# Kernel optimization log

Measured on AMD Instinct MI355X. Metric: run time of the kernel, lower is better.

The kernel has to match this reference:

```python
import math
import jax, jax.numpy as jnp
import numpy as np

T = 4096
D_MODEL = 1024
NUM_HEADS = 16
HEAD_DIM = D_MODEL // NUM_HEADS


def setup_inputs() -> dict:
    key = jax.random.key(0)
    k_x, k_wqkv, k_wproj = jax.random.split(key, 3)
    # match eqx.nn.Linear init scale: U(-1/sqrt(in), 1/sqrt(in)); randn*small works too,
    # but keep magnitudes reasonable so softmax isn't saturated.
    s_in = 1.0 / math.sqrt(D_MODEL)
    x = jax.random.normal(k_x, (T, D_MODEL), dtype=jnp.float32)
    W_qkv = jax.random.normal(k_wqkv, (3 * D_MODEL, D_MODEL), dtype=jnp.float32) * s_in
    b_qkv = jnp.zeros((3 * D_MODEL,), dtype=jnp.float32)
    W_proj = jax.random.normal(k_wproj, (D_MODEL, D_MODEL), dtype=jnp.float32) * s_in
    b_proj = jnp.zeros((D_MODEL,), dtype=jnp.float32)
    return {"x": x, "W_qkv": W_qkv, "b_qkv": b_qkv, "W_proj": W_proj, "b_proj": b_proj}


def reference(x, W_qkv, b_qkv, W_proj, b_proj):
    T_, C = x.shape  # (seq, d_model)
    H, hd = NUM_HEADS, HEAD_DIM
    # c_attn: eqx Linear computes W @ x + b per token -> x @ W.T + b
    qkv = x @ W_qkv.T + b_qkv  # (T, 3C)
    q, k, v = jnp.split(qkv, 3, axis=1)
    # (T, C) -> (H, T, hd)
    q = q.reshape(T_, H, hd).swapaxes(0, 1)
    k = k.reshape(T_, H, hd).swapaxes(0, 1)
    v = v.reshape(T_, H, hd).swapaxes(0, 1)
    scores = jnp.einsum("htd,hsd->hts", q, k) / math.sqrt(hd)  # (H, T, T)
    causal = jnp.tril(jnp.ones((T_, T_), dtype=bool))
    scores = jnp.where(causal, scores, -jnp.inf)
    attn = jax.nn.softmax(scores, axis=-1)
    y = jnp.einsum("hts,hsd->htd", attn, v)  # (H, T, hd)
    y = y.swapaxes(0, 1).reshape(T_, C)
    y = y @ W_proj.T + b_proj
    return y
```

## Files before the change

### kernel.cpp

```cpp
#include <hip/hip_runtime.h>
#include <math.h>
#include <string.h>

#define T_SEQ 4096
#define DM 1024
#define NH 16
#define HD 64

typedef short s8v __attribute__((ext_vector_type(8)));
typedef float f4v __attribute__((ext_vector_type(4)));

__device__ inline unsigned short f2bf(float f) {
    unsigned u; memcpy(&u, &f, 4);
    u = u + 0x7fffu + ((u >> 16) & 1u);
    return (unsigned short)(u >> 16);
}

__device__ inline float bf2f(unsigned short s) {
    unsigned u = (unsigned)s << 16;
    float f; memcpy(&f, &u, 4);
    return f;
}

__device__ inline float exp2fn(float x) {
#if __has_builtin(__builtin_amdgcn_exp2f)
    return __builtin_amdgcn_exp2f(x);
#else
    return exp2f(x);
#endif
}

__device__ inline void gld_lds16(const void* g, void* l) {
    __builtin_amdgcn_global_load_lds(
        (const __attribute__((address_space(1))) void*)g,
        (__attribute__((address_space(3))) void*)l, 16, 0, 0);
}

__global__ __launch_bounds__(256)
void cvt3(const float* __restrict__ i0, unsigned short* __restrict__ o0, int n0,
          const float* __restrict__ i1, unsigned short* __restrict__ o1, int n1,
          const float* __restrict__ i2, unsigned short* __restrict__ o2, int n2) {
    int i = blockIdx.x * 256 + threadIdx.x;
    const float* in; unsigned short* out; int j;
    if (i < n0)           { in = i0; out = o0; j = i; }
    else if (i < n0 + n1) { in = i1; out = o1; j = i - n0; }
    else if (i < n0 + n1 + n2) { in = i2; out = o2; j = i - n0 - n1; }
    else return;
    const float4* p = (const float4*)(in + (size_t)j * 8);
    float4 a = p[0], b = p[1];
    unsigned short o[8] = {f2bf(a.x), f2bf(a.y), f2bf(a.z), f2bf(a.w),
                           f2bf(b.x), f2bf(b.y), f2bf(b.z), f2bf(b.w)};
    uint4 pk; memcpy(&pk, o, 16);
    *(uint4*)(out + (size_t)j * 8) = pk;
}

template<int MODE, int TM, int TN, int WR, int WC>
__global__ __launch_bounds__(WR * WC * 64, 1)
void gemm_tile(const unsigned short* __restrict__ A, const unsigned short* __restrict__ B,
               const float* __restrict__ bias, void* __restrict__ Cout,
               unsigned short* __restrict__ qbuf, unsigned short* __restrict__ kbuf2,
               unsigned short* __restrict__ vT,
               int M, int N, int K, int nbx, int patchw, int patchh) {
    constexpr int W  = WR * WC;
    constexpr int MF = TM / WR / 16;
    constexpr int NF = TN / WC / 16;
    constexpr int NGA = TM / 16, NGB = TN / 16, NG = NGA + NGB;
    __shared__ __align__(16) short As[2][TM * 32];
    __shared__ __align__(16) short Bs[2][TN * 32];
    const int tid = threadIdx.x;
    const int w = tid >> 6, lane = tid & 63;
    const int wr = w / WC, wc = w % WC;
    const int l15 = lane & 15, quad = lane >> 4;

    const int bl = blockIdx.x;
    const int xcd = bl & 7, ii = bl >> 3;
    const int pxn = nbx / patchw;
    const int bx = (xcd % pxn) * patchw + ii % patchw;
    const int by = (xcd / pxn) * patchh + ii / patchw;
    const int m0 = by * TM, n0 = bx * TN;

    f4v acc[MF][NF];
    #pragma unroll
    for (int i = 0; i < MF; ++i)
        #pragma unroll
        for (int j = 0; j < NF; ++j) acc[i][j] = (f4v){0.f, 0.f, 0.f, 0.f};

    auto stage = [&](int buf, int k0) {
        for (int g = w; g < NG; g += W) {
            const unsigned short* src;
            short* dst;
            if (g < NGA) {
                src = A + (size_t)(m0 + g * 16 + l15) * K + quad * 8 + k0;
                dst = &As[buf][g * 512];
            } else {
                src = B + (size_t)(n0 + (g - NGA) * 16 + l15) * K + quad * 8 + k0;
                dst = &Bs[buf][(g - NGA) * 512];
            }
            gld_lds16(src, dst);
        }
    };
    auto compute = [&](int buf) {
        s8v af[MF], bfr[NF];
        #pragma unroll
        for (int i = 0; i < MF; ++i)
            af[i] = *(const s8v*)&As[buf][((wr * MF + i) * 64 + lane) * 8];
        #pragma unroll
        for (int j = 0; j < NF; ++j)
            bfr[j] = *(const s8v*)&Bs[buf][((wc * NF + j) * 64 + lane) * 8];
        #pragma unroll
        for (int i = 0; i < MF; ++i)
            #pragma unroll
            for (int j = 0; j < NF; ++j)
                acc[i][j] = __builtin_amdgcn_mfma_f32_16x16x32_bf16(af[i], bfr[j], acc[i][j], 0, 0, 0);
    };

    stage(0, 0);
    __syncthreads();
    for (int k0 = 0; k0 < K; k0 += 64) {
        stage(1, k0 + 32);
        compute(0);
        __syncthreads();
        if (k0 + 64 < K) stage(0, k0 + 64);
        compute(1);
        __syncthreads();
    }

    float bj[NF];
    #pragma unroll
    for (int j = 0; j < NF; ++j) bj[j] = bias[n0 + wc * (TN / WC) + j * 16 + l15];

    if (MODE == 2) {
        #pragma unroll
        for (int j = 0; j < NF; ++j) {
            const int ccol = n0 + wc * (TN / WC) + j * 16;
            if (ccol >= 2 * DM) {
                const int hh = (ccol - 2 * DM) >> 6;
                const int ob = (ccol & 63) >> 4;
                #pragma unroll
                for (int i = 0; i < MF; ++i) {
                    const int tile = (m0 + wr * (TM / WR)) / 64 + (i >> 2);
                    const int it = i & 3;
                    unsigned short o[4];
                    #pragma unroll
                    for (int rg = 0; rg < 4; ++rg) o[rg] = f2bf(acc[i][j][rg] + bj[j]);
                    unsigned long long pk; memcpy(&pk, o, 8);
                    size_t off = (size_t)hh * 262144 + (size_t)tile * 4096
                               + (size_t)((ob * 2 + (it >> 1)) * 64 + lane) * 8 + (it & 1) * 4;
                    *(unsigned long long*)&vT[off] = pk;
                }
            } else {
                unsigned short* dst = (ccol < DM) ? qbuf : kbuf2;
                const int col = (ccol < DM) ? (ccol + l15) : (ccol - DM + l15);
                #pragma unroll
                for (int i = 0; i < MF; ++i) {
                    #pragma unroll
                    for (int rg = 0; rg < 4; ++rg) {
                        int row = m0 + wr * (TM / WR) + i * 16 + quad * 4 + rg;
                        dst[(size_t)row * DM + col] = f2bf(acc[i][j][rg] + bj[j]);
                    }
                }
            }
        }
    } else {
        #pragma unroll
        for (int i = 0; i < MF; ++i) {
            #pragma unroll
            for (int rg = 0; rg < 4; ++rg) {
                int row = m0 + wr * (TM / WR) + i * 16 + quad * 4 + rg;
                #pragma unroll
                for (int j = 0; j < NF; ++j) {
                    int col = n0 + wc * (TN / WC) + j * 16 + l15;
                    ((float*)Cout)[(size_t)row * N + col] = acc[i][j][rg] + bj[j];
                }
            }
        }
    }
}

__device__ __forceinline__ void soft_step(f4v* st, bool diag, int qloc, int quad,
                                          float& lr, s8v& pf0, s8v& pf1) {
    const float C2  = 0.1803368851f;
    const float MC2 = 12.0f * 0.1803368851f;
    float sv[4][4];
    #pragma unroll
    for (int kb = 0; kb < 4; ++kb)
        #pragma unroll
        for (int rg = 0; rg < 4; ++rg) {
            float s = st[kb][rg];
            if (diag && (kb * 16 + quad * 4 + rg > qloc)) s = -3.0e38f;
            float t = exp2fn(fmaf(s, C2, -MC2));
            sv[kb][rg] = t;
            lr += t;
        }
    int pk[4][2];
    #pragma unroll
    for (int kb = 0; kb < 4; ++kb) {
        unsigned u0 = __float_as_uint(sv[kb][0]) + 0x8000u;
        unsigned u1 = __float_as_uint(sv[kb][1]) + 0x8000u;
        unsigned u2 = __float_as_uint(sv[kb][2]) + 0x8000u;
        unsigned u3 = __float_as_uint(sv[kb][3]) + 0x8000u;
        pk[kb][0] = (int)__builtin_amdgcn_perm(u1, u0, 0x07060302);
        pk[kb][1] = (int)__builtin_amdgcn_perm(u3, u2, 0x07060302);
    }
    int4 a = {pk[0][0], pk[0][1], pk[1][0], pk[1][1]};
    int4 b = {pk[2][0], pk[2][1], pk[3][0], pk[3][1]};
    memcpy(&pf0, &a, 16);
    memcpy(&pf1, &b, 16);
}

__global__ __launch_bounds__(256, 3)
void attn_mfma7(const unsigned short* __restrict__ qb,
                const unsigned short* __restrict__ kbf,
                const unsigned short* __restrict__ vT,
                unsigned short* __restrict__ y0,
                unsigned short* __restrict__ y1,
                unsigned short* __restrict__ y2,
                float* __restrict__ lsum) {
    const int b = blockIdx.x;
    const int par = b % 3;
    const int idx = b / 3;
    const int h = idx & 15, a = idx >> 4;
    const int tid = threadIdx.x;
    const int w = tid >> 6, lane = tid & 63;
    const int quad = lane >> 4, l15 = lane & 15;
    const int cq = h * HD;
    unsigned short* ypar = (par == 0) ? y0 : (par == 1) ? y1 : y2;
    float* lpar = lsum + ((size_t)par * NH + h) * T_SEQ;
    const unsigned short* vbase = vT + (size_t)h * 262144;

    __shared__ short KB[2][4096];
    __shared__ short VTs[2][4096];
    __shared__ short QB[8192];

    for (int ph = 0; ph < 2; ++ph) {
        const int qt = ph ? (31 - a) : a;
        const int q0 = qt * 128;
        const int kmax = 2 * qt + 1;
        const int nk = (kmax >= par) ? (kmax - par) / 3 + 1 : 0;
        const int kt0 = par * 64;

        __syncthreads();
        #pragma unroll
        for (int rr = 0; rr < 4; ++rr) {
            int ch = rr * 256 + tid;
            int qg = ch >> 7, hf = (ch >> 6) & 1, ln = ch & 63;
            gld_lds16(qb + (size_t)(q0 + qg * 16 + (ln & 15)) * DM + cq + hf * 32 + ((ln >> 4) << 3),
                      &QB[(ch & ~63) * 8]);
        }
        if (nk > 0) {
            #pragma unroll
            for (int rr = 0; rr < 2; ++rr) {
                int ch = rr * 256 + tid;
                int blk = ch >> 7, hf = (ch >> 6) & 1, ln = ch & 63;
                gld_lds16(kbf + (size_t)(kt0 + blk * 16 + (ln & 15)) * DM + cq + hf * 32 + ((ln >> 4) << 3),
                          &KB[0][(ch & ~63) * 8]);
                gld_lds16(vbase + (size_t)(kt0 >> 6) * 4096 + (size_t)ch * 8,
                          &VTs[0][(ch & ~63) * 8]);
            }
        }
        __syncthreads();

        s8v qf[2][2];
        #pragma unroll
        for (int g = 0; g < 2; ++g)
            #pragma unroll
            for (int hf = 0; hf < 2; ++hf)
                qf[g][hf] = *(const s8v*)&QB[((((g * 4 + w) * 2 + hf) * 64) + lane) * 8];

        f4v O0[4], O1[4];
        #pragma unroll
        for (int ob = 0; ob < 4; ++ob) {
            O0[ob] = (f4v){0.f, 0.f, 0.f, 0.f};
            O1[ob] = (f4v){0.f, 0.f, 0.f, 0.f};
        }
        float lr0 = 0.f, lr1 = 0.f;

        for (int i = 0; i < nk; ++i) {
            const int kt = par + 3 * i;
            const int p = i & 1;
            const bool g0a = (kt <= 2 * qt);
            const bool m0 = (kt == 2 * qt);
            const bool m1 = (kt == 2 * qt + 1);
            if (i < nk - 1) {
                const int k1 = kt0 + (i + 1) * 192;
                #pragma unroll
                for (int rr = 0; rr < 2; ++rr) {
                    int ch = rr * 256 + tid;
                    int blk = ch >> 7, hf = (ch >> 6) & 1, ln = ch & 63;
                    gld_lds16(kbf + (size_t)(k1 + blk * 16 + (ln & 15)) * DM + cq
                                  + hf * 32 + ((ln >> 4) << 3),
                              &KB[p ^ 1][(ch & ~63) * 8]);
                    gld_lds16(vbase + (size_t)(k1 >> 6) * 4096 + (size_t)ch * 8,
                              &VTs[p ^ 1][(ch & ~63) * 8]);
                }
            }

            f4v st0[4], st1[4];
            #pragma unroll
            for (int kb = 0; kb < 4; ++kb) {
                s8v k0f = *(const s8v*)&KB[p][((kb * 2 + 0) * 64 + lane) * 8];
                s8v k1f = *(const s8v*)&KB[p][((kb * 2 + 1) * 64 + lane) * 8];
                f4v c1 = (f4v){0.f, 0.f, 0.f, 0.f};
                c1 = __builtin_amdgcn_mfma_f32_16x16x32_bf16(k0f, qf[1][0], c1, 0, 0, 0);
                c1 = __builtin_amdgcn_mfma_f32_16x16x32_bf16(k1f, qf[1][1], c1, 0, 0, 0);
                st1[kb] = c1;
                if (g0a) {
                    f4v c0 = (f4v){0.f, 0.f, 0.f, 0.f};
                    c0 = __builtin_amdgcn_mfma_f32_16x16x32_bf16(k0f, qf[0][0], c0, 0, 0, 0);
                    c0 = __builtin_amdgcn_mfma_f32_16x16x32_bf16(k1f, qf[0][1], c0, 0, 0, 0);
                    st0[kb] = c0;
                }
            }

            s8v pf10, pf11, pf00, pf01;
            soft_step(st1, m1, w * 16 + l15, quad, lr1, pf10, pf11);
            if (g0a) soft_step(st0, m0, w * 16 + l15, quad, lr0, pf00, pf01);

            #pragma unroll
            for (int ob = 0; ob < 4; ++ob) {
                s8v v0f = *(const s8v*)&VTs[p][((ob * 2 + 0) * 64 + lane) * 8];
                s8v v1f = *(const s8v*)&VTs[p][((ob * 2 + 1) * 64 + lane) * 8];
                O1[ob] = __builtin_amdgcn_mfma_f32_16x16x32_bf16(v0f, pf10, O1[ob], 0, 0, 0);
                O1[ob] = __builtin_amdgcn_mfma_f32_16x16x32_bf16(v1f, pf11, O1[ob], 0, 0, 0);
                if (g0a) {
                    O0[ob] = __builtin_amdgcn_mfma_f32_16x16x32_bf16(v0f, pf00, O0[ob], 0, 0, 0);
                    O0[ob] = __builtin_amdgcn_mfma_f32_16x16x32_bf16(v1f, pf01, O0[ob], 0, 0, 0);
                }
            }
            __syncthreads();
        }

        lr0 += __shfl_xor(lr0, 16); lr0 += __shfl_xor(lr0, 32);
        lr1 += __shfl_xor(lr1, 16); lr1 += __shfl_xor(lr1, 32);
        #pragma unroll
        for (int g = 0; g < 2; ++g) {
            const f4v* O = g ? O1 : O0;
            int qrow = q0 + g * 64 + w * 16 + l15;
            size_t ybase = (size_t)qrow * DM + cq;
            #pragma unroll
            for (int ob = 0; ob < 4; ++ob) {
                unsigned short o[4];
                #pragma unroll
                for (int rg = 0; rg < 4; ++rg) o[rg] = f2bf(O[ob][rg]);
                unsigned long long pk; memcpy(&pk, o, 8);
                *(unsigned long long*)&ypar[ybase + ob * 16 + quad * 4] = pk;
            }
            if (quad == 0) lpar[qrow] = g ? lr1 : lr0;
        }
    }
}

__global__ __launch_bounds__(256)
void attn_combine3(const unsigned short* __restrict__ y0,
                   const unsigned short* __restrict__ y1,
                   const unsigned short* __restrict__ y2,
                   const float* __restrict__ lsum,
                   unsigned short* __restrict__ yout) {
    int i = blockIdx.x * 256 + threadIdx.x;
    int t = i >> 7, d8 = i & 127;
    int h = d8 >> 3;
    float l = lsum[(size_t)h * T_SEQ + t]
            + lsum[((size_t)NH + h) * T_SEQ + t]
            + lsum[((size_t)2 * NH + h) * T_SEQ + t];
    float inv = 1.f / l;
    size_t off = (size_t)t * DM + d8 * 8;
    uint4 ua = *(const uint4*)(y0 + off);
    uint4 ub = *(const uint4*)(y1 + off);
    uint4 uc = *(const uint4*)(y2 + off);
    const unsigned short* pa = (const unsigned short*)&ua;
    const unsigned short* pb = (const unsigned short*)&ub;
    const unsigned short* pc = (const unsigned short*)&uc;
    unsigned short o[8];
    #pragma unroll
    for (int k = 0; k < 8; ++k)
        o[k] = f2bf((bf2f(pa[k]) + bf2f(pb[k]) + bf2f(pc[k])) * inv);
    uint4 pk; memcpy(&pk, o, 16);
    *(uint4*)(yout + off) = pk;
}

extern "C" void kernel_launch(void* const* d_in, const int* in_sizes, int n_in,
                              void* d_out, int out_size, void* d_ws, size_t ws_size,
                              hipStream_t stream) {
    const float* x     = (const float*)d_in[0];
    const float* Wqkv  = (const float*)d_in[1];
    const float* bqkv  = (const float*)d_in[2];
    const float* Wproj = (const float*)d_in[3];
    const float* bproj = (const float*)d_in[4];
    float* out = (float*)d_out;

    char* ws = (char*)d_ws;
    unsigned short* qbuf  = (unsigned short*)(ws);
    unsigned short* kbuf  = (unsigned short*)(ws + ( 8u << 20));
    unsigned short* vTb   = (unsigned short*)(ws + (16u << 20));
    unsigned short* yattb = (unsigned short*)(ws + (24u << 20));
    unsigned short* wprjb = (unsigned short*)(ws + (32u << 20));
    float*          lsum  = (float*)         (ws + (34u << 20));
    unsigned short* xb    = (unsigned short*)(ws + (35u << 20));
    unsigned short* wqkvb = (unsigned short*)(ws + (43u << 20));
    unsigned short* y0p   = (unsigned short*)(ws + (35u << 20));
    unsigned short* y1p   = (unsigned short*)(ws + (43u << 20));
    unsigned short* y2p   = (unsigned short*)(ws + (51u << 20));

    {
        int n0 = T_SEQ * DM / 8, n1 = 3 * DM * DM / 8, n2 = DM * DM / 8;
        cvt3<<<dim3((n0 + n1 + n2 + 255) / 256), dim3(256), 0, stream>>>(
            x, xb, n0, Wqkv, wqkvb, n1, Wproj, wprjb, n2);
    }
    gemm_tile<2, 256, 192, 2, 4><<<dim3(256), dim3(512), 0, stream>>>(
        xb, wqkvb, bqkv, nullptr, qbuf, kbuf, vTb, T_SEQ, 3 * DM, DM, 16, 8, 4);
    attn_mfma7<<<dim3(768), dim3(256), 0, stream>>>(qbuf, kbuf, vTb, y0p, y1p, y2p, lsum);
    attn_combine3<<<dim3(T_SEQ * DM / 8 / 256), dim3(256), 0, stream>>>(y0p, y1p, y2p, lsum, yattb);
    gemm_tile<0, 128, 128, 2, 2><<<dim3(256), dim3(256), 0, stream>>>(
        yattb, wprjb, bproj, out, nullptr, nullptr, nullptr, T_SEQ, DM, DM, 8, 4, 8);
}
```

Before: 214.5 us.

## Restructure GEMM into triple-buffered four-phase pipeline with explicit waitcnt scheduling

Replaces the double-buffered GEMM main loop with a three-stage LDS ring. Each K-step is split into four phases, and in each phase every wave issues one global-to-LDS load for step s+2 while running a slice of its MFMAs. Explicit vmcnt/lgkmcnt waits, s_barrier, sched_barrier and setprio replace the generic __syncthreads, so loads overlap more deeply with math. The QKV GEMM tile also grows to 256x256 (192 blocks instead of 256), and occupancy hints change. This uses more LDS and barriers per step, and depends on hand-tuned wait counts being correct.

Measured after the change: 222.9 us. 3.9% more time.

```diff
diff --git a/kernel.cpp b/kernel.cpp
--- a/kernel.cpp
+++ b/kernel.cpp
@@ -54,19 +54,22 @@
     *(uint4*)(out + (size_t)j * 8) = pk;
 }
 
-template<int MODE, int TM, int TN, int WR, int WC>
-__global__ __launch_bounds__(WR * WC * 64, 1)
-void gemm_tile(const unsigned short* __restrict__ A, const unsigned short* __restrict__ B,
-               const float* __restrict__ bias, void* __restrict__ Cout,
-               unsigned short* __restrict__ qbuf, unsigned short* __restrict__ kbuf2,
-               unsigned short* __restrict__ vT,
-               int M, int N, int K, int nbx, int patchw, int patchh) {
+template<int MODE, int TM, int TN, int WR, int WC, int OCC>
+__global__ __launch_bounds__(WR * WC * 64, OCC)
+void gemm_8ph(const unsigned short* __restrict__ A, const unsigned short* __restrict__ B,
+              const float* __restrict__ bias, void* __restrict__ Cout,
+              unsigned short* __restrict__ qbuf, unsigned short* __restrict__ kbuf2,
+              unsigned short* __restrict__ vT,
+              int M, int N, int K, int nbx, int patchw, int patchh) {
     constexpr int W  = WR * WC;
     constexpr int MF = TM / WR / 16;
     constexpr int NF = TN / WC / 16;
-    constexpr int NGA = TM / 16, NGB = TN / 16, NG = NGA + NGB;
-    __shared__ __align__(16) short As[2][TM * 32];
-    __shared__ __align__(16) short Bs[2][TN * 32];
+    constexpr int MFP = MF / 4;
+    constexpr int NGA = TM / 16, NGB = TN / 16;
+    static_assert(NGA + NGB == 4 * W, "one stage-load per wave per phase");
+    static_assert(MF % 4 == 0, "4 phases per K-step");
+    __shared__ __align__(16) short As[3][NGA * 512];
+    __shared__ __align__(16) short Bs[3][NGB * 512];
     const int tid = threadIdx.x;
     const int w = tid >> 6, lane = tid & 63;
     const int wr = w / WC, wc = w % WC;
@@ -85,44 +88,54 @@
         #pragma unroll
         for (int j = 0; j < NF; ++j) acc[i][j] = (f4v){0.f, 0.f, 0.f, 0.f};
 
-    auto stage = [&](int buf, int k0) {
-        for (int g = w; g < NG; g += W) {
-            const unsigned short* src;
-            short* dst;
-            if (g < NGA) {
-                src = A + (size_t)(m0 + g * 16 + l15) * K + quad * 8 + k0;
-                dst = &As[buf][g * 512];
-            } else {
-                src = B + (size_t)(n0 + (g - NGA) * 16 + l15) * K + quad * 8 + k0;
-                dst = &Bs[buf][(g - NGA) * 512];
-            }
-            gld_lds16(src, dst);
-        }
+    auto stage_group = [&](int buf, int g, int k0) {
+        if (g < NGA)
+            gld_lds16(A + (size_t)(m0 + g * 16 + l15) * K + quad * 8 + k0,
+                      &As[buf][g * 512]);
+        else
+            gld_lds16(B + (size_t)(n0 + (g - NGA) * 16 + l15) * K + quad * 8 + k0,
+                      &Bs[buf][(g - NGA) * 512]);
     };
-    auto compute = [&](int buf) {
-        s8v af[MF], bfr[NF];
-        #pragma unroll
-        for (int i = 0; i < MF; ++i)
-            af[i] = *(const s8v*)&As[buf][((wr * MF + i) * 64 + lane) * 8];
-        #pragma unroll
-        for (int j = 0; j < NF; ++j)
-            bfr[j] = *(const s8v*)&Bs[buf][((wc * NF + j) * 64 + lane) * 8];
-        #pragma unroll
-        for (int i = 0; i < MF; ++i)
-            #pragma unroll
-            for (int j = 0; j < NF; ++j)
-                acc[i][j] = __builtin_amdgcn_mfma_f32_16x16x32_bf16(af[i], bfr[j], acc[i][j], 0, 0, 0);
-    };
-
-    stage(0, 0);
-    __syncthreads();
-    for (int k0 = 0; k0 < K; k0 += 64) {
-        stage(1, k0 + 32);
-        compute(0);
-        __syncthreads();
-        if (k0 + 64 < K) stage(0, k0 + 64);
-        compute(1);
-        __syncthreads();
+
+    const int nstep = K >> 5;
+    #pragma unroll
+    for (int s = 0; s < 2; ++s)
+        #pragma unroll
+        for (int p = 0; p < 4; ++p)
+            stage_group(s, p * W + w, s * 32);
+
+    for (int s = 0; s < nstep; ++s) {
+        const int cb = s % 3, pb = (s + 2) % 3;
+        if (s + 1 < nstep) asm volatile("s_waitcnt vmcnt(4)" ::: "memory");
+        else               asm volatile("s_waitcnt vmcnt(0)" ::: "memory");
+        __builtin_amdgcn_s_barrier();
+        asm volatile("" ::: "memory");
+        s8v bfr[NF];
+        #pragma unroll
+        for (int p = 0; p < 4; ++p) {
+            if (s + 2 < nstep) stage_group(pb, p * W + w, (s + 2) * 32);
+            s8v af[MFP];
+            #pragma unroll
+            for (int i = 0; i < MFP; ++i)
+                af[i] = *(const s8v*)&As[cb][((wr * MF + p * MFP + i) * 64 + lane) * 8];
+            if (p == 0) {
+                #pragma unroll
+                for (int j = 0; j < NF; ++j)
+                    bfr[j] = *(const s8v*)&Bs[cb][((wc * NF + j) * 64 + lane) * 8];
+            }
+            asm volatile("s_waitcnt lgkmcnt(0)" ::: "memory");
+            __builtin_amdgcn_sched_barrier(0);
+            __builtin_amdgcn_s_setprio(1);
+            #pragma unroll
+            for (int i = 0; i < MFP; ++i)
+                #pragma unroll
+                for (int j = 0; j < NF; ++j)
+                    acc[p * MFP + i][j] = __builtin_amdgcn_mfma_f32_16x16x32_bf16(
+                        af[i], bfr[j], acc[p * MFP + i][j], 0, 0, 0);
+            __builtin_amdgcn_s_setprio(0);
+            __builtin_amdgcn_s_barrier();
+            asm volatile("" ::: "memory");
+        }
     }
 
     float bj[NF];
@@ -406,10 +419,10 @@
         cvt3<<<dim3((n0 + n1 + n2 + 255) / 256), dim3(256), 0, stream>>>(
             x, xb, n0, Wqkv, wqkvb, n1, Wproj, wprjb, n2);
     }
-    gemm_tile<2, 256, 192, 2, 4><<<dim3(256), dim3(512), 0, stream>>>(
-        xb, wqkvb, bqkv, nullptr, qbuf, kbuf, vTb, T_SEQ, 3 * DM, DM, 16, 8, 4);
+    gemm_8ph<2, 256, 256, 2, 4, 2><<<dim3(192), dim3(512), 0, stream>>>(
+        xb, wqkvb, bqkv, nullptr, qbuf, kbuf, vTb, T_SEQ, 3 * DM, DM, 12, 6, 4);
     attn_mfma7<<<dim3(768), dim3(256), 0, stream>>>(qbuf, kbuf, vTb, y0p, y1p, y2p, lsum);
     attn_combine3<<<dim3(T_SEQ * DM / 8 / 256), dim3(256), 0, stream>>>(y0p, y1p, y2p, lsum, yattb);
-    gemm_tile<0, 128, 128, 2, 2><<<dim3(256), dim3(256), 0, stream>>>(
+    gemm_8ph<0, 128, 128, 2, 2, 3><<<dim3(256), dim3(256), 0, stream>>>(
         yattb, wprjb, bproj, out, nullptr, nullptr, nullptr, T_SEQ, DM, DM, 8, 4, 8);
 }
```

## Fuse attention partial combine and normalization into output projection GEMM A-load

Applied to the files above, without the earlier changes.

Removes the separate combine kernel that summed three partial attention outputs and divided by the summed softmax denominators. The projection GEMM, in a new MODE 3, instead stages all three partial A tiles into LDS and forms the combined, normalized bf16 fragment before each MFMA. The per-row denominators are read once per 64-wide k-step, which lines up with one head because HD is 64. This drops a kernel launch and a full write and re-read of the combined activation. In exchange the GEMM triples its A loads and A-side LDS, and adds VALU work to its inner loop, repeated for every column tile.

After: 246.9 us. 1.15x slower.

```diff
diff --git a/kernel.cpp b/kernel.cpp
--- a/kernel.cpp
+++ b/kernel.cpp
@@ -56,7 +56,9 @@
 
 template<int MODE, int TM, int TN, int WR, int WC>
 __global__ __launch_bounds__(WR * WC * 64, 1)
-void gemm_tile(const unsigned short* __restrict__ A, const unsigned short* __restrict__ B,
+void gemm_tile(const unsigned short* __restrict__ A, const unsigned short* __restrict__ A1,
+               const unsigned short* __restrict__ A2, const float* __restrict__ lsm,
+               const unsigned short* __restrict__ B,
                const float* __restrict__ bias, void* __restrict__ Cout,
                unsigned short* __restrict__ qbuf, unsigned short* __restrict__ kbuf2,
                unsigned short* __restrict__ vT,
@@ -65,8 +67,9 @@
     constexpr int MF = TM / WR / 16;
     constexpr int NF = TN / WC / 16;
     constexpr int NGA = TM / 16, NGB = TN / 16, NG = NGA + NGB;
-    __shared__ __align__(16) short As[2][TM * 32];
-    __shared__ __align__(16) short Bs[2][TN * 32];
+    constexpr int NP = (MODE == 3) ? 3 : 1;
+    __shared__ __align__(16) short As[2][NP][NGA * 512];
+    __shared__ __align__(16) short Bs[2][NGB * 512];
     const int tid = threadIdx.x;
     const int w = tid >> 6, lane = tid & 63;
     const int wr = w / WC, wc = w % WC;
@@ -87,23 +90,36 @@
 
     auto stage = [&](int buf, int k0) {
         for (int g = w; g < NG; g += W) {
-            const unsigned short* src;
-            short* dst;
             if (g < NGA) {
-                src = A + (size_t)(m0 + g * 16 + l15) * K + quad * 8 + k0;
-                dst = &As[buf][g * 512];
+                size_t off = (size_t)(m0 + g * 16 + l15) * K + quad * 8 + k0;
+                gld_lds16(A + off, &As[buf][0][g * 512]);
+                if (MODE == 3) {
+                    gld_lds16(A1 + off, &As[buf][1][g * 512]);
+                    gld_lds16(A2 + off, &As[buf][2][g * 512]);
+                }
             } else {
-                src = B + (size_t)(n0 + (g - NGA) * 16 + l15) * K + quad * 8 + k0;
-                dst = &Bs[buf][(g - NGA) * 512];
-            }
-            gld_lds16(src, dst);
+                gld_lds16(B + (size_t)(n0 + (g - NGA) * 16 + l15) * K + quad * 8 + k0,
+                          &Bs[buf][(g - NGA) * 512]);
+            }
         }
     };
-    auto compute = [&](int buf) {
+    auto compute = [&](int buf, const float* inv) {
         s8v af[MF], bfr[NF];
         #pragma unroll
-        for (int i = 0; i < MF; ++i)
-            af[i] = *(const s8v*)&As[buf][((wr * MF + i) * 64 + lane) * 8];
+        for (int i = 0; i < MF; ++i) {
+            if (MODE == 3) {
+                const unsigned short* p0 = (const unsigned short*)&As[buf][0][((wr * MF + i) * 64 + lane) * 8];
+                const unsigned short* p1 = (const unsigned short*)&As[buf][1][((wr * MF + i) * 64 + lane) * 8];
+                const unsigned short* p2 = (const unsigned short*)&As[buf][2][((wr * MF + i) * 64 + lane) * 8];
+                unsigned short o[8];
+                #pragma unroll
+                for (int e = 0; e < 8; ++e)
+                    o[e] = f2bf((bf2f(p0[e]) + bf2f(p1[e]) + bf2f(p2[e])) * inv[i]);
+                memcpy(&af[i], o, 16);
+            } else {
+                af[i] = *(const s8v*)&As[buf][0][((wr * MF + i) * 64 + lane) * 8];
+            }
+        }
         #pragma unroll
         for (int j = 0; j < NF; ++j)
             bfr[j] = *(const s8v*)&Bs[buf][((wc * NF + j) * 64 + lane) * 8];
@@ -117,11 +133,23 @@
     stage(0, 0);
     __syncthreads();
     for (int k0 = 0; k0 < K; k0 += 64) {
+        float inv[MF];
+        if (MODE == 3) {
+            const int hk = k0 >> 6;
+            #pragma unroll
+            for (int i = 0; i < MF; ++i) {
+                int row = m0 + (wr * MF + i) * 16 + l15;
+                float l = lsm[((size_t)(0 * NH + hk)) * T_SEQ + row]
+                        + lsm[((size_t)(1 * NH + hk)) * T_SEQ + row]
+                        + lsm[((size_t)(2 * NH + hk)) * T_SEQ + row];
+                inv[i] = 1.f / l;
+            }
+        }
         stage(1, k0 + 32);
-        compute(0);
+        compute(0, inv);
         __syncthreads();
         if (k0 + 64 < K) stage(0, k0 + 64);
-        compute(1);
+        compute(1, inv);
         __syncthreads();
     }
 
@@ -350,34 +378,6 @@
     }
 }
 
-__global__ __launch_bounds__(256)
-void attn_combine3(const unsigned short* __restrict__ y0,
-                   const unsigned short* __restrict__ y1,
-                   const unsigned short* __restrict__ y2,
-                   const float* __restrict__ lsum,
-                   unsigned short* __restrict__ yout) {
-    int i = blockIdx.x * 256 + threadIdx.x;
-    int t = i >> 7, d8 = i & 127;
-    int h = d8 >> 3;
-    float l = lsum[(size_t)h * T_SEQ + t]
-            + lsum[((size_t)NH + h) * T_SEQ + t]
-            + lsum[((size_t)2 * NH + h) * T_SEQ + t];
-    float inv = 1.f / l;
-    size_t off = (size_t)t * DM + d8 * 8;
-    uint4 ua = *(const uint4*)(y0 + off);
-    uint4 ub = *(const uint4*)(y1 + off);
-    uint4 uc = *(const uint4*)(y2 + off);
-    const unsigned short* pa = (const unsigned short*)&ua;
-    const unsigned short* pb = (const unsigned short*)&ub;
-    const unsigned short* pc = (const unsigned short*)&uc;
-    unsigned short o[8];
-    #pragma unroll
-    for (int k = 0; k < 8; ++k)
-        o[k] = f2bf((bf2f(pa[k]) + bf2f(pb[k]) + bf2f(pc[k])) * inv);
-    uint4 pk; memcpy(&pk, o, 16);
-    *(uint4*)(yout + off) = pk;
-}
-
 extern "C" void kernel_launch(void* const* d_in, const int* in_sizes, int n_in,
                               void* d_out, int out_size, void* d_ws, size_t ws_size,
                               hipStream_t stream) {
@@ -392,7 +392,6 @@
     unsigned short* qbuf  = (unsigned short*)(ws);
     unsigned short* kbuf  = (unsigned short*)(ws + ( 8u << 20));
     unsigned short* vTb   = (unsigned short*)(ws + (16u << 20));
-    unsigned short* yattb = (unsigned short*)(ws + (24u << 20));
     unsigned short* wprjb = (unsigned short*)(ws + (32u << 20));
     float*          lsum  = (float*)         (ws + (34u << 20));
     unsigned short* xb    = (unsigned short*)(ws + (35u << 20));
@@ -407,9 +406,10 @@
             x, xb, n0, Wqkv, wqkvb, n1, Wproj, wprjb, n2);
     }
     gemm_tile<2, 256, 192, 2, 4><<<dim3(256), dim3(512), 0, stream>>>(
-        xb, wqkvb, bqkv, nullptr, qbuf, kbuf, vTb, T_SEQ, 3 * DM, DM, 16, 8, 4);
+        xb, nullptr, nullptr, nullptr, wqkvb, bqkv, nullptr,
+        qbuf, kbuf, vTb, T_SEQ, 3 * DM, DM, 16, 8, 4);
     attn_mfma7<<<dim3(768), dim3(256), 0, stream>>>(qbuf, kbuf, vTb, y0p, y1p, y2p, lsum);
-    attn_combine3<<<dim3(T_SEQ * DM / 8 / 256), dim3(256), 0, stream>>>(y0p, y1p, y2p, lsum, yattb);
-    gemm_tile<0, 128, 128, 2, 2><<<dim3(256), dim3(256), 0, stream>>>(
-        yattb, wprjb, bproj, out, nullptr, nullptr, nullptr, T_SEQ, DM, DM, 8, 4, 8);
-}
+    gemm_tile<3, 128, 128, 2, 2><<<dim3(256), dim3(256), 0, stream>>>(
+        y0p, y1p, y2p, lsum, wprjb, bproj, out,
+        nullptr, nullptr, nullptr, T_SEQ, DM, DM, 8, 4, 8);
+}
```

## Split attention KV range into two partitions with 8-wave blocks

Applied to the files above, without the earlier changes.

Changes the split-K attention from three key-tile partitions with 256-thread blocks (each wave handling two 16-row query groups) to two partitions with 512-thread blocks, where each of 8 waves owns one 16-row query group. Each block now strides key tiles by 2 instead of 3, and the combine kernel sums two partial outputs instead of three. The intent is to reduce partial-output traffic and combine work while keeping per-wave register pressure lower. The trade-off is fewer blocks, a longer serial key loop per block, and idle waves on masked diagonal tiles.

After: 212.2 us (median of 2 runs). About the same (-1.0%).

```diff
diff --git a/kernel.cpp b/kernel.cpp
--- a/kernel.cpp
+++ b/kernel.cpp
@@ -208,23 +208,22 @@
     memcpy(&pf1, &b, 16);
 }
 
-__global__ __launch_bounds__(256, 3)
-void attn_mfma7(const unsigned short* __restrict__ qb,
-                const unsigned short* __restrict__ kbf,
-                const unsigned short* __restrict__ vT,
-                unsigned short* __restrict__ y0,
-                unsigned short* __restrict__ y1,
-                unsigned short* __restrict__ y2,
-                float* __restrict__ lsum) {
+__global__ __launch_bounds__(512, 4)
+void attn_mfma2p(const unsigned short* __restrict__ qb,
+                 const unsigned short* __restrict__ kbf,
+                 const unsigned short* __restrict__ vT,
+                 unsigned short* __restrict__ y0,
+                 unsigned short* __restrict__ y1,
+                 float* __restrict__ lsum) {
     const int b = blockIdx.x;
-    const int par = b % 3;
-    const int idx = b / 3;
+    const int par = b >> 8;
+    const int idx = b & 255;
     const int h = idx & 15, a = idx >> 4;
     const int tid = threadIdx.x;
     const int w = tid >> 6, lane = tid & 63;
     const int quad = lane >> 4, l15 = lane & 15;
     const int cq = h * HD;
-    unsigned short* ypar = (par == 0) ? y0 : (par == 1) ? y1 : y2;
+    unsigned short* ypar = par ? y1 : y0;
     float* lpar = lsum + ((size_t)par * NH + h) * T_SEQ;
     const unsigned short* vbase = vT + (size_t)h * 262144;
 
@@ -232,148 +231,118 @@
     __shared__ short VTs[2][4096];
     __shared__ short QB[8192];
 
+    const bool lo = (w < 4);
+    const int qloc = (w & 3) * 16 + l15;
+
     for (int ph = 0; ph < 2; ++ph) {
         const int qt = ph ? (31 - a) : a;
         const int q0 = qt * 128;
-        const int kmax = 2 * qt + 1;
-        const int nk = (kmax >= par) ? (kmax - par) / 3 + 1 : 0;
+        const int nk = qt + 1;
         const int kt0 = par * 64;
 
         __syncthreads();
         #pragma unroll
-        for (int rr = 0; rr < 4; ++rr) {
-            int ch = rr * 256 + tid;
+        for (int rr = 0; rr < 2; ++rr) {
+            int ch = rr * 512 + tid;
             int qg = ch >> 7, hf = (ch >> 6) & 1, ln = ch & 63;
             gld_lds16(qb + (size_t)(q0 + qg * 16 + (ln & 15)) * DM + cq + hf * 32 + ((ln >> 4) << 3),
                       &QB[(ch & ~63) * 8]);
         }
-        if (nk > 0) {
+        {
+            int ch = tid;
+            int blk = ch >> 7, hf = (ch >> 6) & 1, ln = ch & 63;
+            gld_lds16(kbf + (size_t)(kt0 + blk * 16 + (ln & 15)) * DM + cq + hf * 32 + ((ln >> 4) << 3),
+                      &KB[0][(ch & ~63) * 8]);
+            gld_lds16(vbase + (size_t)(kt0 >> 6) * 4096 + (size_t)ch * 8,
+                      &VTs[0][(ch & ~63) * 8]);
+        }
+        __syncthreads();
+
+        s8v qf[2];
+        #pragma unroll
+        for (int hf = 0; hf < 2; ++hf)
+            qf[hf] = *(const s8v*)&QB[(((w * 2 + hf) * 64) + lane) * 8];
+
+        f4v O[4];
+        #pragma unroll
+        for (int ob = 0; ob < 4; ++ob) O[ob] = (f4v){0.f, 0.f, 0.f, 0.f};
+        float lr = 0.f;
+
+        for (int i = 0; i < nk; ++i) {
+            const int kt = par + 2 * i;
+            const int p = i & 1;
+            const bool diag = lo ? (kt == 2 * qt) : (kt == 2 * qt + 1);
+            const bool skip = lo && (kt == 2 * qt + 1);
+            if (i < nk - 1) {
+                const int k1 = kt0 + (i + 1) * 128;
+                int ch = tid;
+                int blk = ch >> 7, hf = (ch >> 6) & 1, ln = ch & 63;
+                gld_lds16(kbf + (size_t)(k1 + blk * 16 + (ln & 15)) * DM + cq
+                              + hf * 32 + ((ln >> 4) << 3),
+                          &KB[p ^ 1][(ch & ~63) * 8]);
+                gld_lds16(vbase + (size_t)(k1 >> 6) * 4096 + (size_t)ch * 8,
+                          &VTs[p ^ 1][(ch & ~63) * 8]);
+            }
+
+            if (!skip) {
+                f4v st[4];
+                #pragma unroll
+                for (int kb = 0; kb < 4; ++kb) {
+                    s8v k0f = *(const s8v*)&KB[p][((kb * 2 + 0) * 64 + lane) * 8];
+                    s8v k1f = *(const s8v*)&KB[p][((kb * 2 + 1) * 64 + lane) * 8];
+                    f4v c = (f4v){0.f, 0.f, 0.f, 0.f};
+                    c = __builtin_amdgcn_mfma_f32_16x16x32_bf16(k0f, qf[0], c, 0, 0, 0);
+                    c = __builtin_amdgcn_mfma_f32_16x16x32_bf16(k1f, qf[1], c, 0, 0, 0);
+                    st[kb] = c;
+                }
+                s8v pf0, pf1;
+                soft_step(st, diag, qloc, quad, lr, pf0, pf1);
+                #pragma unroll
+                for (int ob = 0; ob < 4; ++ob) {
+                    s8v v0f = *(const s8v*)&VTs[p][((ob * 2 + 0) * 64 + lane) * 8];
+                    s8v v1f = *(const s8v*)&VTs[p][((ob * 2 + 1) * 64 + lane) * 8];
+                    O[ob] = __builtin_amdgcn_mfma_f32_16x16x32_bf16(v0f, pf0, O[ob], 0, 0, 0);
+                    O[ob] = __builtin_amdgcn_mfma_f32_16x16x32_bf16(v1f, pf1, O[ob], 0, 0, 0);
+                }
+            }
+            __syncthreads();
+        }
+
+        lr += __shfl_xor(lr, 16); lr += __shfl_xor(lr, 32);
+        const int qrow = q0 + w * 16 + l15;
+        const size_t ybase = (size_t)qrow * DM + cq;
+        #pragma unroll
+        for (int ob = 0; ob < 4; ++ob) {
+            unsigned short o[4];
             #pragma unroll
-            for (int rr = 0; rr < 2; ++rr) {
-                int ch = rr * 256 + tid;
-                int blk = ch >> 7, hf = (ch >> 6) & 1, ln = ch & 63;
-                gld_lds16(kbf + (size_t)(kt0 + blk * 16 + (ln & 15)) * DM + cq + hf * 32 + ((ln >> 4) << 3),
-                          &KB[0][(ch & ~63) * 8]);
-                gld_lds16(vbase + (size_t)(kt0 >> 6) * 4096 + (size_t)ch * 8,
-                          &VTs[0][(ch & ~63) * 8]);
-            }
-        }
-        __syncthreads();
-
-        s8v qf[2][2];
-        #pragma unroll
-        for (int g = 0; g < 2; ++g)
-            #pragma unroll
-            for (int hf = 0; hf < 2; ++hf)
-                qf[g][hf] = *(const s8v*)&QB[((((g * 4 + w) * 2 + hf) * 64) + lane) * 8];
-
-        f4v O0[4], O1[4];
-        #pragma unroll
-        for (int ob = 0; ob < 4; ++ob) {
-            O0[ob] = (f4v){0.f, 0.f, 0.f, 0.f};
-            O1[ob] = (f4v){0.f, 0.f, 0.f, 0.f};
-        }
-        float lr0 = 0.f, lr1 = 0.f;
-
-        for (int i = 0; i < nk; ++i) {
-            const int kt = par + 3 * i;
-            const int p = i & 1;
-            const bool g0a = (kt <= 2 * qt);
-            const bool m0 = (kt == 2 * qt);
-            const bool m1 = (kt == 2 * qt + 1);
-            if (i < nk - 1) {
-                const int k1 = kt0 + (i + 1) * 192;
-                #pragma unroll
-                for (int rr = 0; rr < 2; ++rr) {
-                    int ch = rr * 256 + tid;
-                    int blk = ch >> 7, hf = (ch >> 6) & 1, ln = ch & 63;
-                    gld_lds16(kbf + (size_t)(k1 + blk * 16 + (ln & 15)) * DM + cq
-                                  + hf * 32 + ((ln >> 4) << 3),
-                              &KB[p ^ 1][(ch & ~63) * 8]);
-                    gld_lds16(vbase + (size_t)(k1 >> 6) * 4096 + (size_t)ch * 8,
-                              &VTs[p ^ 1][(ch & ~63) * 8]);
-                }
-            }
-
-            f4v st0[4], st1[4];
-            #pragma unroll
-            for (int kb = 0; kb < 4; ++kb) {
-                s8v k0f = *(const s8v*)&KB[p][((kb * 2 + 0) * 64 + lane) * 8];
-                s8v k1f = *(const s8v*)&KB[p][((kb * 2 + 1) * 64 + lane) * 8];
-                f4v c1 = (f4v){0.f, 0.f, 0.f, 0.f};
-                c1 = __builtin_amdgcn_mfma_f32_16x16x32_bf16(k0f, qf[1][0], c1, 0, 0, 0);
-                c1 = __builtin_amdgcn_mfma_f32_16x16x32_bf16(k1f, qf[1][1], c1, 0, 0, 0);
-                st1[kb] = c1;
-                if (g0a) {
-                    f4v c0 = (f4v){0.f, 0.f, 0.f, 0.f};
-                    c0 = __builtin_amdgcn_mfma_f32_16x16x32_bf16(k0f, qf[0][0], c0, 0, 0, 0);
-                    c0 = __builtin_amdgcn_mfma_f32_16x16x32_bf16(k1f, qf[0][1], c0, 0, 0, 0);
-                    st0[kb] = c0;
-                }
-            }
-
-            s8v pf10, pf11, pf00, pf01;
-            soft_step(st1, m1, w * 16 + l15, quad, lr1, pf10, pf11);
-            if (g0a) soft_step(st0, m0, w * 16 + l15, quad, lr0, pf00, pf01);
-
-            #pragma unroll
-            for (int ob = 0; ob < 4; ++ob) {
-                s8v v0f = *(const s8v*)&VTs[p][((ob * 2 + 0) * 64 + lane) * 8];
-                s8v v1f = *(const s8v*)&VTs[p][((ob * 2 + 1) * 64 + lane) * 8];
-                O1[ob] = __builtin_amdgcn_mfma_f32_16x16x32_bf16(v0f, pf10, O1[ob], 0, 0, 0);
-                O1[ob] = __builtin_amdgcn_mfma_f32_16x16x32_bf16(v1f, pf11, O1[ob], 0, 0, 0);
-                if (g0a) {
-                    O0[ob] = __builtin_amdgcn_mfma_f32_16x16x32_bf16(v0f, pf00, O0[ob], 0, 0, 0);
-                    O0[ob] = __builtin_amdgcn_mfma_f32_16x16x32_bf16(v1f, pf01, O0[ob], 0, 0, 0);
-                }
-            }
-            __syncthreads();
-        }
-
-        lr0 += __shfl_xor(lr0, 16); lr0 += __shfl_xor(lr0, 32);
-        lr1 += __shfl_xor(lr1, 16); lr1 += __shfl_xor(lr1, 32);
-        #pragma unroll
-        for (int g = 0; g < 2; ++g) {
-            const f4v* O = g ? O1 : O0;
-            int qrow = q0 + g * 64 + w * 16 + l15;
-            size_t ybase = (size_t)qrow * DM + cq;
-            #pragma unroll
-            for (int ob = 0; ob < 4; ++ob) {
-                unsigned short o[4];
-                #pragma unroll
-                for (int rg = 0; rg < 4; ++rg) o[rg] = f2bf(O[ob][rg]);
-                unsigned long long pk; memcpy(&pk, o, 8);
-                *(unsigned long long*)&ypar[ybase + ob * 16 + quad * 4] = pk;
-            }
-            if (quad == 0) lpar[qrow] = g ? lr1 : lr0;
-        }
+            for (int rg = 0; rg < 4; ++rg) o[rg] = f2bf(O[ob][rg]);
+            unsigned long long pk; memcpy(&pk, o, 8);
+            *(unsigned long long*)&ypar[ybase + ob * 16 + quad * 4] = pk;
+        }
+        if (quad == 0) lpar[qrow] = lr;
     }
 }
 
 __global__ __launch_bounds__(256)
-void attn_combine3(const unsigned short* __restrict__ y0,
+void attn_combine2(const unsigned short* __restrict__ y0,
                    const unsigned short* __restrict__ y1,
-                   const unsigned short* __restrict__ y2,
                    const float* __restrict__ lsum,
                    unsigned short* __restrict__ yout) {
     int i = blockIdx.x * 256 + threadIdx.x;
     int t = i >> 7, d8 = i & 127;
     int h = d8 >> 3;
     float l = lsum[(size_t)h * T_SEQ + t]
-            + lsum[((size_t)NH + h) * T_SEQ + t]
-            + lsum[((size_t)2 * NH + h) * T_SEQ + t];
+            + lsum[((size_t)NH + h) * T_SEQ + t];
     float inv = 1.f / l;
     size_t off = (size_t)t * DM + d8 * 8;
     uint4 ua = *(const uint4*)(y0 + off);
     uint4 ub = *(const uint4*)(y1 + off);
-    uint4 uc = *(const uint4*)(y2 + off);
     const unsigned short* pa = (const unsigned short*)&ua;
     const unsigned short* pb = (const unsigned short*)&ub;
-    const unsigned short* pc = (const unsigned short*)&uc;
     unsigned short o[8];
     #pragma unroll
     for (int k = 0; k < 8; ++k)
-        o[k] = f2bf((bf2f(pa[k]) + bf2f(pb[k]) + bf2f(pc[k])) * inv);
+        o[k] = f2bf((bf2f(pa[k]) + bf2f(pb[k])) * inv);
     uint4 pk; memcpy(&pk, o, 16);
     *(uint4*)(yout + off) = pk;
 }
@@ -399,7 +368,6 @@
     unsigned short* wqkvb = (unsigned short*)(ws + (43u << 20));
     unsigned short* y0p   = (unsigned short*)(ws + (35u << 20));
     unsigned short* y1p   = (unsigned short*)(ws + (43u << 20));
-    unsigned short* y2p   = (unsigned short*)(ws + (51u << 20));
 
     {
         int n0 = T_SEQ * DM / 8, n1 = 3 * DM * DM / 8, n2 = DM * DM / 8;
@@ -408,8 +376,8 @@
     }
     gemm_tile<2, 256, 192, 2, 4><<<dim3(256), dim3(512), 0, stream>>>(
         xb, wqkvb, bqkv, nullptr, qbuf, kbuf, vTb, T_SEQ, 3 * DM, DM, 16, 8, 4);
-    attn_mfma7<<<dim3(768), dim3(256), 0, stream>>>(qbuf, kbuf, vTb, y0p, y1p, y2p, lsum);
-    attn_combine3<<<dim3(T_SEQ * DM / 8 / 256), dim3(256), 0, stream>>>(y0p, y1p, y2p, lsum, yattb);
+    attn_mfma2p<<<dim3(512), dim3(512), 0, stream>>>(qbuf, kbuf, vTb, y0p, y1p, lsum);
+    attn_combine2<<<dim3(T_SEQ * DM / 8 / 256), dim3(256), 0, stream>>>(y0p, y1p, lsum, yattb);
     gemm_tile<0, 128, 128, 2, 2><<<dim3(256), dim3(256), 0, stream>>>(
         yattb, wprjb, bproj, out, nullptr, nullptr, nullptr, T_SEQ, DM, DM, 8, 4, 8);
 }
```
